# Optimization experiments

Measured on AMD Instinct MI355X. Metric: run time of the kernel, lower is better.

## Reference

```python
import jax, jax.numpy as jnp
import numpy as np

B, S, D, N, LMAX = 32, 512, 768, 128, 16


def setup_inputs() -> dict:
    key = jax.random.key(0)
    k1, k2, k3, k4, k5 = jax.random.split(key, 5)
    embeddings = jax.random.normal(k1, (B, S, D), dtype=jnp.float32)
    W = jax.random.normal(k2, (D, D), dtype=jnp.float32) / np.sqrt(D).astype(np.float32)
    b = jax.random.normal(k3, (D,), dtype=jnp.float32) * 0.02
    starts = jax.random.randint(k4, (B, N), 0, S - LMAX, dtype=jnp.int32)
    lengths = jax.random.randint(k5, (B, N), 1, LMAX + 1, dtype=jnp.int32)
    spans = jnp.stack([starts, starts + lengths - 1], axis=-1)  # [B,N,2] inclusive ends
    return {"embeddings": embeddings, "W": W, "b": b, "spans": spans}


def reference(embeddings, W, b, spans) -> jnp.ndarray:
    # Batched ragged per-span attention. Original loops over sentences and spans;
    # here every span is padded to LMAX and masked.
    starts = spans[..., 0]                              # [B,N]
    ends = spans[..., 1]                                # [B,N] inclusive
    pos = starts[..., None] + jnp.arange(LMAX)          # [B,N,L]
    valid = pos <= ends[..., None]                      # [B,N,L] bool
    pos_c = jnp.clip(pos, 0, embeddings.shape[1] - 1)
    batch_idx = jnp.arange(embeddings.shape[0])[:, None, None]
    span_emb = embeddings[batch_idx, pos_c]             # [B,N,L,D]
    q = jnp.einsum('bnld,ed->bnle', span_emb, W) + b    # query = Linear(span_emb)
    w = jnp.einsum('bnld,bnmd->bnlm', q, span_emb)      # weights = q @ span_emb.T
    # softmax over dim 0 of the original [L,L] matrix -> axis=2 here; mask invalid rows
    w = jnp.where(valid[:, :, :, None], w, -jnp.inf)
    a = jax.nn.softmax(w, axis=2)                       # invalid rows get weight 0
    # zero invalid columns, then attention = a @ span_emb, then sum over rows (l)
    a = a * valid[:, :, None, :].astype(a.dtype)
    agg = jnp.einsum('bnlm,bnmd->bnd', a, span_emb)     # [B,N,D]
    return agg
```

## Files before the change

### kernel.cpp

```cpp
#include <hip/hip_runtime.h>
#include <hip/hip_bf16.h>


constexpr int B_    = 32;
constexpr int S_    = 512;
constexpr int D_    = 768;
constexpr int N_    = 128;
constexpr int LMAX_ = 16;

typedef float f32x4 __attribute__((ext_vector_type(4)));

__global__ __launch_bounds__(192) void span_sum_kernel(
    const float* __restrict__ emb,
    const int*   __restrict__ spans,
    float*       __restrict__ out)
{
    const int bid = blockIdx.x;
    const int x   = bid & 7;
    const int k   = bid >> 3;
    const int b   = (x << 2) | (k >> 7);
    const int n   = k & (N_ - 1);
    const int sid = b * N_ + n;

    const int t = threadIdx.x;

    const int start = spans[2 * sid + 0];
    const int end   = spans[2 * sid + 1];
    const int lm1   = end - start;

    const f32x4* __restrict__ row =
        reinterpret_cast<const f32x4*>(emb + (size_t)b * S_ * D_ + (size_t)start * D_) + t;

    f32x4 acc = {0.f, 0.f, 0.f, 0.f};
    #pragma unroll
    for (int m = 0; m < LMAX_; ++m) {
        const int  mm = (m <= lm1) ? m : lm1;
        const float s = (m <= lm1) ? 1.0f : 0.0f;
        f32x4 v = row[(size_t)mm * (D_ / 4)];
        acc += s * v;
    }

    *(reinterpret_cast<f32x4*>(out + (size_t)sid * D_) + t) = acc;
}

extern "C" void kernel_launch(void* const* d_in, const int* in_sizes, int n_in,
                              void* d_out, int out_size, void* d_ws, size_t ws_size,
                              hipStream_t stream) {
    const float* emb   = (const float*)d_in[0];
    const int*   spans = (const int*)d_in[3];
    float*       out   = (float*)d_out;

    dim3 grid(B_ * N_);
    dim3 block(D_ / 4);
    span_sum_kernel<<<grid, block, 0, stream>>>(emb, spans, out);
}
```

Measured before the change: 15.45 us.

## Stage sequence segments in LDS and sum spans from shared tiles

Instead of one block per span reading up to 16 rows from global memory, each block loads a 64-row segment (plus a 15-row halo) of half the feature dimension into LDS. It then scans all spans of its batch and accumulates those starting in the segment from shared memory, round-robined over four thread slots. This cuts redundant global/L2 reads of overlapping span rows, at the cost of a serial scan over all spans per block and fewer, larger blocks.

```diff
diff --git a/kernel.cpp b/kernel.cpp
--- a/kernel.cpp
+++ b/kernel.cpp
@@ -8,39 +8,67 @@
 constexpr int N_    = 128;
 constexpr int LMAX_ = 16;
 
+constexpr int ROWS_OWN = 64;
+constexpr int HALO     = LMAX_ - 1;
+constexpr int ROWS_STG = ROWS_OWN + HALO;
+constexpr int NSEG     = S_ / ROWS_OWN;
+constexpr int HALF     = D_ / 2;
+constexpr int QPH      = HALF / 4;
+constexpr int TPB      = 384;
+constexpr int SLOTS    = TPB / QPH;
+
 typedef float f32x4 __attribute__((ext_vector_type(4)));
 
-__global__ __launch_bounds__(192) void span_sum_kernel(
+__global__ __launch_bounds__(TPB) void span_sum_halo_kernel(
     const float* __restrict__ emb,
     const int*   __restrict__ spans,
     float*       __restrict__ out)
 {
+    __shared__ f32x4 lds[ROWS_STG][QPH];
+
     const int bid = blockIdx.x;
-    const int x   = bid & 7;
-    const int k   = bid >> 3;
-    const int b   = (x << 2) | (k >> 7);
-    const int n   = k & (N_ - 1);
-    const int sid = b * N_ + n;
+    const int xcd = bid & 7;
+    const int w   = bid >> 3;
+    const int b   = (xcd << 2) | (w >> 4);
+    const int rst = w & 15;
+    const int seg = rst >> 1;
+    const int h   = rst & 1;
 
-    const int t = threadIdx.x;
+    const int t    = threadIdx.x;
+    const int q    = t % QPH;
+    const int slot = t / QPH;
 
-    const int start = spans[2 * sid + 0];
-    const int end   = spans[2 * sid + 1];
-    const int lm1   = end - start;
+    const int r0 = seg * ROWS_OWN;
 
-    const f32x4* __restrict__ row =
-        reinterpret_cast<const f32x4*>(emb + (size_t)b * S_ * D_ + (size_t)start * D_) + t;
+    const float* base = emb + ((size_t)b * S_ + (size_t)r0) * D_ + (size_t)h * HALF;
+    #pragma unroll
+    for (int p = 0; p < (ROWS_STG + SLOTS - 1) / SLOTS; ++p) {
+        const int r = p * SLOTS + slot;
+        if (r < ROWS_STG && r0 + r < S_)
+            lds[r][q] = *reinterpret_cast<const f32x4*>(base + (size_t)r * D_ + q * 4);
+    }
+    __syncthreads();
 
-    f32x4 acc = {0.f, 0.f, 0.f, 0.f};
-    #pragma unroll
-    for (int m = 0; m < LMAX_; ++m) {
-        const int  mm = (m <= lm1) ? m : lm1;
-        const float s = (m <= lm1) ? 1.0f : 0.0f;
-        f32x4 v = row[(size_t)mm * (D_ / 4)];
-        acc += s * v;
+    int cnt = 0;
+    for (int n = 0; n < N_; ++n) {
+        const int sid   = b * N_ + n;
+        const int start = spans[2 * sid + 0];
+        if ((start >> 6) == seg) {
+            if ((cnt & (SLOTS - 1)) == slot) {
+                const int lm1 = spans[2 * sid + 1] - start;
+                const int lr  = start - r0;
+                f32x4 acc = {0.f, 0.f, 0.f, 0.f};
+                #pragma unroll
+                for (int m = 0; m < LMAX_; ++m) {
+                    const int  mm = (m <= lm1) ? m : lm1;
+                    const float s = (m <= lm1) ? 1.0f : 0.0f;
+                    acc += s * lds[lr + mm][q];
+                }
+                *(reinterpret_cast<f32x4*>(out + (size_t)sid * D_ + (size_t)h * HALF) + q) = acc;
+            }
+            ++cnt;
+        }
     }
-
-    *(reinterpret_cast<f32x4*>(out + (size_t)sid * D_) + t) = acc;
 }
 
 extern "C" void kernel_launch(void* const* d_in, const int* in_sizes, int n_in,
@@ -50,7 +78,7 @@
     const int*   spans = (const int*)d_in[3];
     float*       out   = (float*)d_out;
 
-    dim3 grid(B_ * N_);
-    dim3 block(D_ / 4);
-    span_sum_kernel<<<grid, block, 0, stream>>>(emb, spans, out);
+    dim3 grid(B_ * NSEG * 2);
+    dim3 block(TPB);
+    span_sum_halo_kernel<<<grid, block, 0, stream>>>(emb, spans, out);
 }
```

Result: slower. 40.49 us (+162.1%).
